# Performance work log

Measured on AMD Instinct MI355X. Metric: run time of the kernel, lower is better.

## Reference

```python
import jax, jax.numpy as jnp
import numpy as np

B, S, D_IN, D_OUT = 16, 2048, 512, 64
N_SLOTS = 1000  # faithful to original kernel shape; only slices 0..2 used
SCALE = 1.0 / jnp.sqrt(jnp.float32(64.0))


def setup_inputs() -> dict:
    key = jax.random.key(0)
    k1, k2 = jax.random.split(key)
    inputs = jax.random.normal(k1, (B, S, D_IN), dtype=jnp.float32)
    # keras 'uniform' initializer: U(-0.05, 0.05)
    kernel = jax.random.uniform(k2, (N_SLOTS, D_IN, D_OUT), dtype=jnp.float32,
                                minval=-0.05, maxval=0.05)
    return {"inputs": inputs, "kernel": kernel}


def reference(inputs, kernel):
    # Q, K, V projections: [B,S,D_in] @ [D_in,D_out] -> [B,S,D_out]
    q = jnp.einsum('bsi,io->bso', inputs, kernel[0])
    k = jnp.einsum('bsi,io->bso', inputs, kernel[1])
    v = jnp.einsum('bsi,io->bso', inputs, kernel[2])
    # scores: [B,S,S], scaled by 1/sqrt(64)
    scores = jnp.einsum('bqd,bkd->bqk', q, k) * SCALE
    attn = jax.nn.softmax(scores, axis=-1)
    # output: [B,S,D_out]
    return jnp.einsum('bqk,bkd->bqd', attn, v)
```

## Files before the change

### kernel.cpp

```cpp
#include <hip/hip_runtime.h>
#include <hip/hip_bf16.h>

typedef __bf16 bhalf;
typedef __attribute__((ext_vector_type(8)))  __bf16 bhalf8;
typedef __attribute__((ext_vector_type(4)))  float  f32x4;
typedef __attribute__((ext_vector_type(16))) float  f32x16;
typedef __attribute__((ext_vector_type(4)))  unsigned int u32x4;

#define NB   16
#define SEQ  2048
#define DIN  512
#define DOUT 64
#define NTOK (NB*SEQ)
#define NSPLIT 4
#define KVPER (SEQ/NSPLIT)

#define WT_BYTES (192*512*2)
#define Q_OFF    ((size_t)WT_BYTES)
#define QKV_BYTES ((size_t)NTOK*DOUT*2)
#define K_OFF    (Q_OFF + QKV_BYTES)
#define VT_OFF   (K_OFF + QKV_BYTES)

__device__ __forceinline__ void gl_lds16(const void* g, void* l) {
  __builtin_amdgcn_global_load_lds(
      (const __attribute__((address_space(1))) void*)g,
      (__attribute__((address_space(3))) void*)l, 16, 0, 0);
}

__global__ __launch_bounds__(256) void prep_w(const float* __restrict__ wk,
                                              bhalf* __restrict__ wt) {
  int tid  = blockIdx.x*256 + threadIdx.x;
  int slot = tid >> 15;
  int rem  = tid & 32767;
  int k    = rem >> 6;
  int col  = rem & 63;
  float v  = wk[tid];
  if (slot == 0) v *= 0.18033688011112042f;
  wt[(size_t)(slot*64 + col)*DIN + k] = (bhalf)v;
}

__global__ __launch_bounds__(512) void proj_qkv(const float* __restrict__ x,
    const bhalf* __restrict__ wt, bhalf* __restrict__ qb,
    bhalf* __restrict__ kb, bhalf* __restrict__ vtb) {
  __shared__ __align__(16) char smem[81920];
  char* const xs  = smem;
  char* const wsl = smem + 32768;

  const int tid  = threadIdx.x;
  const int lane = tid & 63;
  const int wv   = tid >> 6;
  const int tg   = wv & 3;
  const int ng   = wv >> 2;
  const int r16  = lane & 15;
  const int g    = lane >> 4;
  const int tok0 = blockIdx.x * 64;

  const char* const xg = (const char*)(x + (size_t)tok0 * DIN);
  const char* const wg = (const char*)wt;

  auto stage = [&](int buf, int c) {
#pragma unroll
    for (int i = 0; i < 5; ++i) {
      const int p = wv*5 + i;
      if (p < 24) {
        const int n = p*8 + (lane >> 3);
        const int s = lane & 7;
        gl_lds16(wg + (size_t)n*1024 + c*128 + ((s ^ (n & 7)) << 4),
                 wsl + buf*24576 + p*1024);
      } else {
        const int q = p - 24;
        const int r = q*4 + (lane >> 4);
        const int s = lane & 15;
        gl_lds16(xg + (size_t)r*2048 + c*256 + ((s ^ (r & 7)) << 4),
                 xs + buf*16384 + q*1024);
      }
    }
  };

  f32x4 acc0 = {0.f,0.f,0.f,0.f}, acc1 = acc0, acc2 = acc0,
        acc3 = acc0, acc4 = acc0, acc5 = acc0;

  stage(0, 0);
  __syncthreads();

  const int row = tg*16 + r16;
  const int rx7 = r16 & 7;

  int buf = 0;
  for (int c = 0; c < 8; ++c) {
    if (c < 7) stage(buf ^ 1, c + 1);
    const char* xrow = xs  + buf*16384 + row*256;
    const char* wb   = wsl + buf*24576;
#pragma unroll
    for (int kk = 0; kk < 2; ++kk) {
      const int sa = kk*8 + g*2;
      f32x4 xa = *(const f32x4*)(xrow + (( sa      ^ rx7) << 4));
      f32x4 xc = *(const f32x4*)(xrow + (((sa + 1) ^ rx7) << 4));
      bhalf8 a;
      a[0]=(bhalf)xa[0]; a[1]=(bhalf)xa[1]; a[2]=(bhalf)xa[2]; a[3]=(bhalf)xa[3];
      a[4]=(bhalf)xc[0]; a[5]=(bhalf)xc[1]; a[6]=(bhalf)xc[2]; a[7]=(bhalf)xc[3];
      const int sb = (kk*4 + g) ^ rx7;
      __builtin_amdgcn_s_setprio(1);
#define MF(J, ACC) do {                                                         \
        const int nt_ = ng*6 + (J);                                             \
        const bhalf8 bf_ = *(const bhalf8*)(wb + (nt_*16 + r16)*128 + (sb << 4)); \
        ACC = __builtin_amdgcn_mfma_f32_16x16x32_bf16(a, bf_, ACC, 0, 0, 0);    \
      } while (0)
      MF(0, acc0); MF(1, acc1); MF(2, acc2);
      MF(3, acc3); MF(4, acc4); MF(5, acc5);
#undef MF
      __builtin_amdgcn_s_setprio(0);
    }
    __syncthreads();
    buf ^= 1;
  }

#define STOREJ(J, ACC) do {                                                     \
    const int nt = ng*6 + (J);                                                  \
    if (nt < 8) {                                                               \
      bhalf* dst = (nt < 4) ? qb : kb;                                          \
      const size_t base = (size_t)(nt & 3)*512 + (size_t)(r16 >> 3)*256 + (r16 & 7); \
      _Pragma("unroll")                                                         \
      for (int rr = 0; rr < 4; ++rr) {                                          \
        const int tok = tok0 + tg*16 + g*4 + rr;                                \
        dst[(size_t)(tok >> 5)*2048 + base + (tok & 31)*8] = (bhalf)ACC[rr];    \
      }                                                                         \
    } else {                                                                    \
      _Pragma("unroll")                                                         \
      for (int rr = 0; rr < 4; ++rr)                                            \
        vlds[tg][(nt - 8)*16 + r16][g*4 + rr] = (bhalf)ACC[rr];                 \
    } } while (0)

  auto vlds = (bhalf(*)[64][24])(void*)smem;
  STOREJ(0, acc0); STOREJ(1, acc1); STOREJ(2, acc2);
  STOREJ(3, acc3); STOREJ(4, acc4); STOREJ(5, acc5);
#undef STOREJ
  __syncthreads();
  if (ng == 1) {
    const int f    = lane;
    const int tokG = tok0 + tg*16;
    const int tile = tokG >> 5;
    const int s    = (tokG >> 4) & 1;
    bhalf8 v0 = *(const bhalf8*)&vlds[tg][f][0];
    bhalf8 v1 = *(const bhalf8*)&vlds[tg][f][8];
    bhalf* dstv = vtb + (size_t)tile*2048 + (size_t)(f >> 5)*1024
                      + (size_t)s*512 + (size_t)(f & 31)*8;
    *(bhalf8*)dstv         = v0;
    *(bhalf8*)(dstv + 256) = v1;
  }
}

__device__ __forceinline__ unsigned cvtpk(float lo, float hi_) {
  unsigned r;
  asm("v_cvt_pk_bf16_f32 %0, %1, %2" : "=v"(r) : "v"(lo), "v"(hi_));
  return r;
}
__device__ __forceinline__ bhalf8 mk8(unsigned a, unsigned b, unsigned c, unsigned d) {
  u32x4 u; u[0]=a; u[1]=b; u[2]=c; u[3]=d;
  return __builtin_bit_cast(bhalf8, u);
}

__global__ __launch_bounds__(256) void attn(const bhalf* __restrict__ qb,
    const bhalf* __restrict__ kb, const bhalf* __restrict__ vtb,
    float* __restrict__ out) {
  __shared__ float po[NSPLIT][64][33];
  __shared__ float pl[NSPLIT][32];

  const int lane = threadIdx.x & 63;
  const int wv   = threadIdx.x >> 6;
  const int l31  = lane & 31;
  const int hi   = lane >> 5;

  const int pr    = (blockIdx.x & 7)*64 + (blockIdx.x >> 3);
  const int qtA   = pr*2;
  const int qtB   = qtA + 1;
  const int b     = qtA >> 6;
  const int tile0 = b*64 + wv*16;
  const int fo    = hi*256 + l31*8;

  const bhalf* qpA = qb + (size_t)qtA*2048 + fo;
  const bhalf8 qfA0 = *(const bhalf8*)(qpA);
  const bhalf8 qfA1 = *(const bhalf8*)(qpA + 512);
  const bhalf8 qfA2 = *(const bhalf8*)(qpA + 1024);
  const bhalf8 qfA3 = *(const bhalf8*)(qpA + 1536);
  const bhalf* qpB = qb + (size_t)qtB*2048 + fo;
  const bhalf8 qfB0 = *(const bhalf8*)(qpB);
  const bhalf8 qfB1 = *(const bhalf8*)(qpB + 512);
  const bhalf8 qfB2 = *(const bhalf8*)(qpB + 1024);
  const bhalf8 qfB3 = *(const bhalf8*)(qpB + 1536);

  const bhalf* kpk = kb  + (size_t)tile0*2048 + fo;
  const bhalf* vpk = vtb + (size_t)tile0*2048 + fo;

  f32x16 otA0, otA1, otB0, otB1;
#pragma unroll
  for (int r = 0; r < 16; ++r) { otA0[r]=0.f; otA1[r]=0.f; otB0[r]=0.f; otB1[r]=0.f; }
  float lsA = 0.f, lsB = 0.f;

  bhalf8 kf0, kf1, kf2, kf3;
  bhalf8 vf0, vf1, vf2, vf3;
  bhalf8 pfA0, pfA1, pfB0, pfB1;
  f32x16 s;

#define LOADK(IT) do { const bhalf* p_ = kpk + (IT)*2048;                       \
    kf0 = *(const bhalf8*)(p_);          kf1 = *(const bhalf8*)(p_ + 512);      \
    kf2 = *(const bhalf8*)(p_ + 1024);   kf3 = *(const bhalf8*)(p_ + 1536); } while (0)
#define LOADV(IT) do { const bhalf* p_ = vpk + (IT)*2048;                       \
    vf0 = *(const bhalf8*)(p_);          vf1 = *(const bhalf8*)(p_ + 512);      \
    vf2 = *(const bhalf8*)(p_ + 1024);   vf3 = *(const bhalf8*)(p_ + 1536); } while (0)
#define QK(QF0, QF1, QF2, QF3) do {                                             \
    _Pragma("unroll") for (int r_ = 0; r_ < 16; ++r_) s[r_] = 0.f;              \
    __builtin_amdgcn_s_setprio(1);                                              \
    s = __builtin_amdgcn_mfma_f32_32x32x16_bf16(kf0, QF0, s, 0, 0, 0);          \
    s = __builtin_amdgcn_mfma_f32_32x32x16_bf16(kf1, QF1, s, 0, 0, 0);          \
    s = __builtin_amdgcn_mfma_f32_32x32x16_bf16(kf2, QF2, s, 0, 0, 0);          \
    s = __builtin_amdgcn_mfma_f32_32x32x16_bf16(kf3, QF3, s, 0, 0, 0);          \
    __builtin_amdgcn_s_setprio(0); } while (0)
#define SM(PF0, PF1, LS) do {                                                   \
    _Pragma("unroll") for (int r_ = 0; r_ < 16; ++r_)                           \
      s[r_] = __builtin_amdgcn_exp2f(s[r_]);                                    \
    LS += ((s[0]+s[1])+(s[2]+s[3])) + ((s[4]+s[5])+(s[6]+s[7]))                 \
        + ((s[8]+s[9])+(s[10]+s[11])) + ((s[12]+s[13])+(s[14]+s[15]));          \
    unsigned w0 = cvtpk(s[0],  s[1]),  w1 = cvtpk(s[2],  s[3]);                 \
    unsigned w2 = cvtpk(s[4],  s[5]),  w3 = cvtpk(s[6],  s[7]);                 \
    unsigned w4 = cvtpk(s[8],  s[9]),  w5 = cvtpk(s[10], s[11]);                \
    unsigned w6 = cvtpk(s[12], s[13]), w7 = cvtpk(s[14], s[15]);                \
    asm volatile("v_permlane32_swap_b32 %0, %1" : "+v"(w0), "+v"(w2));          \
    asm volatile("v_permlane32_swap_b32 %0, %1" : "+v"(w1), "+v"(w3));          \
    asm volatile("v_permlane32_swap_b32 %0, %1" : "+v"(w4), "+v"(w6));          \
    asm volatile("v_permlane32_swap_b32 %0, %1" : "+v"(w5), "+v"(w7));          \
    PF0 = mk8(w0, w1, w2, w3);                                                  \
    PF1 = mk8(w4, w5, w6, w7); } while (0)
#define PV(PF0, PF1, OT0, OT1) do {                                             \
    __builtin_amdgcn_s_setprio(1);                                              \
    OT0 = __builtin_amdgcn_mfma_f32_32x32x16_bf16(vf0, PF0, OT0, 0, 0, 0);      \
    OT0 = __builtin_amdgcn_mfma_f32_32x32x16_bf16(vf1, PF1, OT0, 0, 0, 0);      \
    OT1 = __builtin_amdgcn_mfma_f32_32x32x16_bf16(vf2, PF0, OT1, 0, 0, 0);      \
    OT1 = __builtin_amdgcn_mfma_f32_32x32x16_bf16(vf3, PF1, OT1, 0, 0, 0);      \
    __builtin_amdgcn_s_setprio(0); } while (0)

  LOADK(0);
  LOADV(0);

  for (int it = 0; it < KVPER/32; ++it) {
    QK(qfA0, qfA1, qfA2, qfA3);
    SM(pfA0, pfA1, lsA);
    QK(qfB0, qfB1, qfB2, qfB3);
    if (it < KVPER/32 - 1) LOADK(it + 1);
    PV(pfA0, pfA1, otA0, otA1);
    SM(pfB0, pfB1, lsB);
    PV(pfB0, pfB1, otB0, otB1);
    if (it < KVPER/32 - 1) LOADV(it + 1);
  }

#undef LOADK
#undef LOADV
#undef QK
#undef SM
#undef PV

  lsA += __shfl_xor(lsA, 32);
  lsB += __shfl_xor(lsB, 32);

#pragma unroll
  for (int r = 0; r < 16; ++r) {
    int d0 = (r & 3) + 8*(r >> 2) + 4*hi;
    po[wv][d0][l31]      = otA0[r];
    po[wv][32 + d0][l31] = otA1[r];
  }
  if (hi == 0) pl[wv][l31] = lsA;
  __syncthreads();
  {
    int q  = threadIdx.x >> 3;
    int dg = (threadIdx.x & 7) * 8;
    float L   = pl[0][q] + pl[1][q] + pl[2][q] + pl[3][q];
    float inv = 1.0f / L;
    float* orow = out + (size_t)(qtA*32 + q)*DOUT + dg;
#pragma unroll
    for (int j = 0; j < 8; ++j)
      orow[j] = (po[0][dg+j][q] + po[1][dg+j][q]
               + po[2][dg+j][q] + po[3][dg+j][q]) * inv;
  }
  __syncthreads();
#pragma unroll
  for (int r = 0; r < 16; ++r) {
    int d0 = (r & 3) + 8*(r >> 2) + 4*hi;
    po[wv][d0][l31]      = otB0[r];
    po[wv][32 + d0][l31] = otB1[r];
  }
  if (hi == 0) pl[wv][l31] = lsB;
  __syncthreads();
  {
    int q  = threadIdx.x >> 3;
    int dg = (threadIdx.x & 7) * 8;
    float L   = pl[0][q] + pl[1][q] + pl[2][q] + pl[3][q];
    float inv = 1.0f / L;
    float* orow = out + (size_t)(qtB*32 + q)*DOUT + dg;
#pragma unroll
    for (int j = 0; j < 8; ++j)
      orow[j] = (po[0][dg+j][q] + po[1][dg+j][q]
               + po[2][dg+j][q] + po[3][dg+j][q]) * inv;
  }
}

extern "C" void kernel_launch(void* const* d_in, const int* in_sizes, int n_in,
                              void* d_out, int out_size, void* d_ws, size_t ws_size,
                              hipStream_t stream) {
  const float* x  = (const float*)d_in[0];
  const float* wk = (const float*)d_in[1];
  float* out = (float*)d_out;

  char* ws = (char*)d_ws;
  bhalf* wt = (bhalf*)(ws);
  bhalf* qq = (bhalf*)(ws + Q_OFF);
  bhalf* kk = (bhalf*)(ws + K_OFF);
  bhalf* vt = (bhalf*)(ws + VT_OFF);

  prep_w  <<<dim3(384), dim3(256), 0, stream>>>(wk, wt);
  proj_qkv<<<dim3(512), dim3(512), 0, stream>>>(x, wt, qq, kk, vt);
  attn    <<<dim3(512), dim3(256), 0, stream>>>(qq, kk, vt, out);
}
```

Baseline: 49.55 us.

## Deepen QKV projection pipeline to 4 LDS buffers with prefetch distance two

Restructures the QKV projection GEMM loop to use 16 smaller K-chunks across four rotating LDS buffers, prefetching two chunks ahead. Full __syncthreads is replaced with explicit partial vmcnt waits plus a raw s_barrier, so global-to-LDS loads overlap with MFMA work on earlier chunks. Weight and activation staging are also split between fixed wave groups. The cost is more barriers per K step and reliance on hand-counted vmcnt values being correct.

```diff
diff --git a/kernel.cpp b/kernel.cpp
--- a/kernel.cpp
+++ b/kernel.cpp
@@ -59,60 +59,73 @@
   const char* const wg = (const char*)wt;
 
   auto stage = [&](int buf, int c) {
-#pragma unroll
-    for (int i = 0; i < 5; ++i) {
-      const int p = wv*5 + i;
-      if (p < 24) {
+    if (wv < 4) {
+#pragma unroll
+      for (int i = 0; i < 3; ++i) {
+        const int p = wv*3 + i;
+        const int n = p*16 + (lane >> 2);
+        const int s = lane & 3;
+        gl_lds16(wg + (size_t)n*1024 + c*64 + ((s ^ (n & 3)) << 4),
+                 wsl + buf*12288 + p*1024);
+      }
+    } else {
+#pragma unroll
+      for (int i = 0; i < 2; ++i) {
+        const int p = (wv - 4)*2 + i;
         const int n = p*8 + (lane >> 3);
         const int s = lane & 7;
-        gl_lds16(wg + (size_t)n*1024 + c*128 + ((s ^ (n & 7)) << 4),
-                 wsl + buf*24576 + p*1024);
-      } else {
-        const int q = p - 24;
-        const int r = q*4 + (lane >> 4);
-        const int s = lane & 15;
-        gl_lds16(xg + (size_t)r*2048 + c*256 + ((s ^ (r & 7)) << 4),
-                 xs + buf*16384 + q*1024);
+        gl_lds16(xg + (size_t)n*2048 + c*128 + ((s ^ (n & 7)) << 4),
+                 xs + buf*8192 + p*1024);
       }
     }
   };
+  auto waitvm = [&](bool deep) {
+    if (wv < 4) {
+      if (deep) asm volatile("s_waitcnt vmcnt(3)" ::: "memory");
+      else      asm volatile("s_waitcnt vmcnt(0)" ::: "memory");
+    } else {
+      if (deep) asm volatile("s_waitcnt vmcnt(2)" ::: "memory");
+      else      asm volatile("s_waitcnt vmcnt(0)" ::: "memory");
+    }
+  };
 
   f32x4 acc0 = {0.f,0.f,0.f,0.f}, acc1 = acc0, acc2 = acc0,
         acc3 = acc0, acc4 = acc0, acc5 = acc0;
 
   stage(0, 0);
-  __syncthreads();
+  stage(1, 1);
+  waitvm(true);
+  __builtin_amdgcn_s_barrier();
+  __builtin_amdgcn_sched_barrier(0);
 
   const int row = tg*16 + r16;
   const int rx7 = r16 & 7;
-
-  int buf = 0;
-  for (int c = 0; c < 8; ++c) {
-    if (c < 7) stage(buf ^ 1, c + 1);
-    const char* xrow = xs  + buf*16384 + row*256;
-    const char* wb   = wsl + buf*24576;
-#pragma unroll
-    for (int kk = 0; kk < 2; ++kk) {
-      const int sa = kk*8 + g*2;
-      f32x4 xa = *(const f32x4*)(xrow + (( sa      ^ rx7) << 4));
-      f32x4 xc = *(const f32x4*)(xrow + (((sa + 1) ^ rx7) << 4));
-      bhalf8 a;
-      a[0]=(bhalf)xa[0]; a[1]=(bhalf)xa[1]; a[2]=(bhalf)xa[2]; a[3]=(bhalf)xa[3];
-      a[4]=(bhalf)xc[0]; a[5]=(bhalf)xc[1]; a[6]=(bhalf)xc[2]; a[7]=(bhalf)xc[3];
-      const int sb = (kk*4 + g) ^ rx7;
-      __builtin_amdgcn_s_setprio(1);
+  const int sbw = (g ^ (r16 & 3)) << 4;
+
+  for (int c = 0; c < 16; ++c) {
+    if (c + 2 < 16) stage((c + 2) & 3, c + 2);
+    const char* xrow = xs + (c & 3)*8192 + row*128;
+    f32x4 xa = *(const f32x4*)(xrow + (((g*2    ) ^ rx7) << 4));
+    f32x4 xc = *(const f32x4*)(xrow + (((g*2 + 1) ^ rx7) << 4));
+    bhalf8 a;
+    a[0]=(bhalf)xa[0]; a[1]=(bhalf)xa[1]; a[2]=(bhalf)xa[2]; a[3]=(bhalf)xa[3];
+    a[4]=(bhalf)xc[0]; a[5]=(bhalf)xc[1]; a[6]=(bhalf)xc[2]; a[7]=(bhalf)xc[3];
+    const char* wb = wsl + (c & 3)*12288;
+    __builtin_amdgcn_s_setprio(1);
 #define MF(J, ACC) do {                                                         \
-        const int nt_ = ng*6 + (J);                                             \
-        const bhalf8 bf_ = *(const bhalf8*)(wb + (nt_*16 + r16)*128 + (sb << 4)); \
-        ACC = __builtin_amdgcn_mfma_f32_16x16x32_bf16(a, bf_, ACC, 0, 0, 0);    \
-      } while (0)
-      MF(0, acc0); MF(1, acc1); MF(2, acc2);
-      MF(3, acc3); MF(4, acc4); MF(5, acc5);
+      const int nt_ = ng*6 + (J);                                               \
+      const bhalf8 bf_ = *(const bhalf8*)(wb + (nt_*16 + r16)*64 + sbw);        \
+      ACC = __builtin_amdgcn_mfma_f32_16x16x32_bf16(a, bf_, ACC, 0, 0, 0);      \
+    } while (0)
+    MF(0, acc0); MF(1, acc1); MF(2, acc2);
+    MF(3, acc3); MF(4, acc4); MF(5, acc5);
 #undef MF
-      __builtin_amdgcn_s_setprio(0);
+    __builtin_amdgcn_s_setprio(0);
+    if (c < 15) {
+      waitvm(c + 2 < 16);
+      __builtin_amdgcn_s_barrier();
+      __builtin_amdgcn_sched_barrier(0);
     }
-    __syncthreads();
-    buf ^= 1;
   }
 
 #define STOREJ(J, ACC) do {                                                     \
```

Result: no change. 50.10 us (+1.1%).

## Halve projection token tile and preload whole x tile as bf16 in LDS

Applied to the files above, without the earlier changes.

The QKV projection block now covers 32 tokens instead of 64, doubling the grid to 1024 blocks, and each wave computes 3 output column tiles instead of 6. The x tile is loaded once up front, converted to bf16 and stored swizzled in LDS, so only the weights are double-buffered per K-chunk and the inner loop no longer converts fp32 to bf16. This aims to raise parallelism and remove repeated per-step conversion work. In exchange, each block re-stages the full weight matrix for half as many tokens, doubling total weight traffic, and the x load is no longer overlapped.

```diff
diff --git a/kernel.cpp b/kernel.cpp
--- a/kernel.cpp
+++ b/kernel.cpp
@@ -43,71 +43,70 @@
     const bhalf* __restrict__ wt, bhalf* __restrict__ qb,
     bhalf* __restrict__ kb, bhalf* __restrict__ vtb) {
   __shared__ __align__(16) char smem[81920];
-  char* const xs  = smem;
+  char* const xls = smem;
   char* const wsl = smem + 32768;
 
   const int tid  = threadIdx.x;
   const int lane = tid & 63;
   const int wv   = tid >> 6;
-  const int tg   = wv & 3;
-  const int ng   = wv >> 2;
+  const int tg   = wv & 1;
+  const int nq   = wv >> 1;
   const int r16  = lane & 15;
   const int g    = lane >> 4;
-  const int tok0 = blockIdx.x * 64;
-
-  const char* const xg = (const char*)(x + (size_t)tok0 * DIN);
+  const int tok0 = blockIdx.x * 32;
+
   const char* const wg = (const char*)wt;
 
-  auto stage = [&](int buf, int c) {
-#pragma unroll
-    for (int i = 0; i < 5; ++i) {
-      const int p = wv*5 + i;
-      if (p < 24) {
-        const int n = p*8 + (lane >> 3);
-        const int s = lane & 7;
-        gl_lds16(wg + (size_t)n*1024 + c*128 + ((s ^ (n & 7)) << 4),
-                 wsl + buf*24576 + p*1024);
-      } else {
-        const int q = p - 24;
-        const int r = q*4 + (lane >> 4);
-        const int s = lane & 15;
-        gl_lds16(xg + (size_t)r*2048 + c*256 + ((s ^ (r & 7)) << 4),
-                 xs + buf*16384 + q*1024);
-      }
+  auto stageW = [&](int buf, int c) {
+#pragma unroll
+    for (int i = 0; i < 3; ++i) {
+      const int p = wv*3 + i;
+      const int n = p*8 + (lane >> 3);
+      const int s = lane & 7;
+      gl_lds16(wg + (size_t)n*1024 + c*128 + ((s ^ (n & 7)) << 4),
+               wsl + buf*24576 + p*1024);
     }
   };
 
-  f32x4 acc0 = {0.f,0.f,0.f,0.f}, acc1 = acc0, acc2 = acc0,
-        acc3 = acc0, acc4 = acc0, acc5 = acc0;
-
-  stage(0, 0);
-  __syncthreads();
+  stageW(0, 0);
+  {
+    const int row = tid >> 4;
+    const int kb8 = (tid & 15) * 8;
+    const float* xr = x + (size_t)(tok0 + row)*DIN + kb8;
+#pragma unroll
+    for (int p = 0; p < 4; ++p) {
+      f32x4 va = *(const f32x4*)(xr + p*128);
+      f32x4 vb = *(const f32x4*)(xr + p*128 + 4);
+      bhalf8 v;
+      v[0]=(bhalf)va[0]; v[1]=(bhalf)va[1]; v[2]=(bhalf)va[2]; v[3]=(bhalf)va[3];
+      v[4]=(bhalf)vb[0]; v[5]=(bhalf)vb[1]; v[6]=(bhalf)vb[2]; v[7]=(bhalf)vb[3];
+      const int slot = ((tid & 15) + 16*p) ^ (row & 7);
+      *(bhalf8*)(xls + row*1024 + slot*16) = v;
+    }
+  }
+  __syncthreads();
+
+  f32x4 acc0 = {0.f,0.f,0.f,0.f}, acc1 = acc0, acc2 = acc0;
 
   const int row = tg*16 + r16;
   const int rx7 = r16 & 7;
 
   int buf = 0;
   for (int c = 0; c < 8; ++c) {
-    if (c < 7) stage(buf ^ 1, c + 1);
-    const char* xrow = xs  + buf*16384 + row*256;
-    const char* wb   = wsl + buf*24576;
+    if (c < 7) stageW(buf ^ 1, c + 1);
+    const char* wb = wsl + buf*24576;
 #pragma unroll
     for (int kk = 0; kk < 2; ++kk) {
-      const int sa = kk*8 + g*2;
-      f32x4 xa = *(const f32x4*)(xrow + (( sa      ^ rx7) << 4));
-      f32x4 xc = *(const f32x4*)(xrow + (((sa + 1) ^ rx7) << 4));
-      bhalf8 a;
-      a[0]=(bhalf)xa[0]; a[1]=(bhalf)xa[1]; a[2]=(bhalf)xa[2]; a[3]=(bhalf)xa[3];
-      a[4]=(bhalf)xc[0]; a[5]=(bhalf)xc[1]; a[6]=(bhalf)xc[2]; a[7]=(bhalf)xc[3];
+      const int o = (c*2 + kk)*4 + g;
+      const bhalf8 a = *(const bhalf8*)(xls + row*1024 + ((o ^ rx7) << 4));
       const int sb = (kk*4 + g) ^ rx7;
       __builtin_amdgcn_s_setprio(1);
 #define MF(J, ACC) do {                                                         \
-        const int nt_ = ng*6 + (J);                                             \
+        const int nt_ = nq*3 + (J);                                             \
         const bhalf8 bf_ = *(const bhalf8*)(wb + (nt_*16 + r16)*128 + (sb << 4)); \
         ACC = __builtin_amdgcn_mfma_f32_16x16x32_bf16(a, bf_, ACC, 0, 0, 0);    \
       } while (0)
       MF(0, acc0); MF(1, acc1); MF(2, acc2);
-      MF(3, acc3); MF(4, acc4); MF(5, acc5);
 #undef MF
       __builtin_amdgcn_s_setprio(0);
     }
@@ -115,8 +114,9 @@
     buf ^= 1;
   }
 
+  auto vlds = (bhalf(*)[64][24])(void*)smem;
 #define STOREJ(J, ACC) do {                                                     \
-    const int nt = ng*6 + (J);                                                  \
+    const int nt = nq*3 + (J);                                                  \
     if (nt < 8) {                                                               \
       bhalf* dst = (nt < 4) ? qb : kb;                                          \
       const size_t base = (size_t)(nt & 3)*512 + (size_t)(r16 >> 3)*256 + (r16 & 7); \
@@ -131,20 +131,16 @@
         vlds[tg][(nt - 8)*16 + r16][g*4 + rr] = (bhalf)ACC[rr];                 \
     } } while (0)
 
-  auto vlds = (bhalf(*)[64][24])(void*)smem;
   STOREJ(0, acc0); STOREJ(1, acc1); STOREJ(2, acc2);
-  STOREJ(3, acc3); STOREJ(4, acc4); STOREJ(5, acc5);
 #undef STOREJ
   __syncthreads();
-  if (ng == 1) {
+  if (wv < 2) {
     const int f    = lane;
-    const int tokG = tok0 + tg*16;
-    const int tile = tokG >> 5;
-    const int s    = (tokG >> 4) & 1;
-    bhalf8 v0 = *(const bhalf8*)&vlds[tg][f][0];
-    bhalf8 v1 = *(const bhalf8*)&vlds[tg][f][8];
+    const int tile = tok0 >> 5;
+    bhalf8 v0 = *(const bhalf8*)&vlds[wv][f][0];
+    bhalf8 v1 = *(const bhalf8*)&vlds[wv][f][8];
     bhalf* dstv = vtb + (size_t)tile*2048 + (size_t)(f >> 5)*1024
-                      + (size_t)s*512 + (size_t)(f & 31)*8;
+                      + (size_t)wv*512 + (size_t)(f & 31)*8;
     *(bhalf8*)dstv         = v0;
     *(bhalf8*)(dstv + 256) = v1;
   }
@@ -316,7 +312,7 @@
   bhalf* kk = (bhalf*)(ws + K_OFF);
   bhalf* vt = (bhalf*)(ws + VT_OFF);
 
-  prep_w  <<<dim3(384), dim3(256), 0, stream>>>(wk, wt);
-  proj_qkv<<<dim3(512), dim3(512), 0, stream>>>(x, wt, qq, kk, vt);
-  attn    <<<dim3(512), dim3(256), 0, stream>>>(qq, kk, vt, out);
-}
+  prep_w  <<<dim3(384),  dim3(256), 0, stream>>>(wk, wt);
+  proj_qkv<<<dim3(1024), dim3(512), 0, stream>>>(x, wt, qq, kk, vt);
+  attn    <<<dim3(512),  dim3(256), 0, stream>>>(qq, kk, vt, out);
+}
```

New measurement: 54.22 us. 1.09x slower.
